# Optimization experiments

Measured on AMD Instinct MI355X. Metric: run time of the kernel, lower is better.

Reference implementation:

```python
import jax, jax.numpy as jnp
import numpy as np

B, N, MA, MB = 8, 16384, 256, 64
K_INTERP, K_AB = 3, 16


def _pn3(x, layers):
    # shared MLP over points: x [B, C, N]
    for w, b in layers:
        x = jax.nn.relu(jnp.einsum('oi,bin->bon', w, x) + b[None, :, None])
    return x


def _pn4(x, layers):
    # shared MLP over (node, neighbor): x [B, C, M, K]
    for w, b in layers:
        x = jax.nn.relu(jnp.einsum('oi,bimk->bomk', w, x) + b[None, :, None, None])
    return x


def _seg_sum(data, ids):  # data [B, N, C], ids [B, N] -> [B, MA, C]
    return jax.vmap(lambda d, i: jax.ops.segment_sum(d, i, num_segments=MA))(data, ids)


def _seg_max(data, ids):  # data [B, N, C], ids [B, N] -> [B, MA, C]
    return jax.vmap(lambda d, i: jax.ops.segment_max(d, i, num_segments=MA))(data, ids)


def _forward(pc, intensity, sn, label, node_a, node_b, *params):
    p = list(params)
    fp1 = [(p[0], p[1]), (p[2], p[3]), (p[4], p[5])]
    fp2 = [(p[6], p[7]), (p[8], p[9])]
    knn1 = [(p[10], p[11]), (p[12], p[13])]
    knn2 = [(p[14], p[15]), (p[16], p[17])]
    fin = [(p[18], p[19]), (p[20], p[21])]

    # ---- point -> node_a assignment (nearest node) ----
    diff = jnp.linalg.norm(pc[:, :, :, None] - node_a[:, :, None, :], axis=1)  # [B, N, MA]
    _, min_k_idx = jax.lax.top_k(-diff, K_INTERP)  # [B, N, k], smallest distances
    min_idx = min_k_idx[:, :, 0]  # [B, N]

    # ---- masked cluster mean (scatter-add by cluster id) ----
    counts = _seg_sum(jnp.ones((B, N, 1), pc.dtype), min_idx)[..., 0]  # [B, MA]
    nonempty = counts > 0  # mask_row_max
    cluster_mean = jnp.swapaxes(_seg_sum(jnp.swapaxes(pc, 1, 2), min_idx), 1, 2) / (counts[:, None, :] + 1e-5)  # [B,3,MA]

    pc_centers = jnp.take_along_axis(cluster_mean, jnp.broadcast_to(min_idx[:, None, :], (B, 3, N)), axis=2)
    pc_decentered = jax.lax.stop_gradient(pc - pc_centers)
    pc_aug = jnp.concatenate([pc_decentered, intensity, sn, label], axis=1)  # [B, 8, N]

    # ---- first PointNet + scatter-max fusion ----
    f1 = _pn3(pc_aug, fp1)  # [B, Ca/2, N]
    m1 = jnp.where(nonempty[:, None, :], jnp.swapaxes(_seg_max(jnp.swapaxes(f1, 1, 2), min_idx), 1, 2), 0.0)  # [B, Ca/2, MA]
    scat1 = jnp.take_along_axis(m1, jnp.broadcast_to(min_idx[:, None, :], (B, m1.shape[1], N)), axis=2)
    f2 = _pn3(jnp.concatenate([f1, scat1], axis=1), fp2)  # [B, Ca, N]
    node_a_features = jnp.where(nonempty[:, None, :], jnp.swapaxes(_seg_max(jnp.swapaxes(f2, 1, 2), min_idx), 1, 2), 0.0)  # [B, Ca, MA]

    # ---- KNN fusion: node_b queries vs cluster means ----
    d2 = jnp.linalg.norm(node_b[:, :, :, None] - cluster_mean[:, :, None, :], axis=1)  # [B, MB, MA]
    _, knn_idx = jax.lax.top_k(-d2, K_AB)  # [B, MB, K]
    pos_knn = jax.vmap(lambda cm, idx: cm[:, idx])(cluster_mean, knn_idx)  # [B, 3, MB, K]
    feat_knn = jax.vmap(lambda f, idx: f[:, idx])(node_a_features, knn_idx)  # [B, Ca, MB, K]
    x = jnp.concatenate([pos_knn - node_b[:, :, :, None], feat_knn], axis=1)  # [B, 3+Ca, MB, K]
    y = _pn4(x, knn1)  # [B, Cb, MB, K]
    pooled = jnp.max(y, axis=3, keepdims=True)
    z = _pn4(jnp.concatenate([jnp.broadcast_to(pooled, y.shape), y], axis=1), knn2)  # [B, Cb, MB, K]
    node_b_features = jnp.max(z, axis=3)  # [B, Cb, MB]

    # ---- final PointNet + global max-pool ----
    final = _pn3(jnp.concatenate([node_b, node_b_features], axis=1), fin)  # [B, Cg, MB]
    global_feature = jnp.max(final, axis=2, keepdims=True)  # [B, Cg, 1]
    return (pc_centers, cluster_mean, min_k_idx, f1, f2, node_a_features, node_b_features, global_feature)


def setup_inputs() -> dict:
    key = jax.random.key(0)
    ks = jax.random.split(key, 32)
    inp = {
        'pc': jax.random.normal(ks[0], (B, 3, N), jnp.float32),
        'intensity': jax.random.uniform(ks[1], (B, 1, N), dtype=jnp.float32),
        'sn': jax.random.normal(ks[2], (B, 3, N), jnp.float32),
        'label': jax.random.uniform(ks[3], (B, 1, N), dtype=jnp.float32),
        'node_a': jax.random.normal(ks[4], (B, 3, MA), jnp.float32),
        'node_b': jax.random.normal(ks[5], (B, 3, MB), jnp.float32),
    }
    i = [6]
    def lin(cin, cout):
        w = jax.random.normal(ks[i[0]], (cout, cin), jnp.float32) / np.sqrt(cin).astype(np.float32)
        i[0] += 1
        return w, jnp.zeros((cout,), jnp.float32)
    for name, dims in [('fp1', [8, 32, 32, 32]), ('fp2', [64, 64, 64]), ('knn1', [67, 256, 256]), ('knn2', [512, 512, 256]), ('fin', [259, 512, 1024])]:
        for j in range(len(dims) - 1):
            w, b = lin(dims[j], dims[j + 1])
            inp[f'{name}_w{j}'] = w
            inp[f'{name}_b{j}'] = b
    return inp


def reference(pc, intensity, sn, label, node_a, node_b, fp1_w0, fp1_b0, fp1_w1, fp1_b1, fp1_w2, fp1_b2, fp2_w0, fp2_b0, fp2_w1, fp2_b1, knn1_w0, knn1_b0, knn1_w1, knn1_b1, knn2_w0, knn2_b0, knn2_w1, knn2_b1, fin_w0, fin_b0, fin_w1, fin_b1):
    return _forward(pc, intensity, sn, label, node_a, node_b, fp1_w0, fp1_b0, fp1_w1, fp1_b1, fp1_w2, fp1_b2, fp2_w0, fp2_b0, fp2_w1, fp2_b1, knn1_w0, knn1_b0, knn1_w1, knn1_b1, knn2_w0, knn2_b0, knn2_w1, knn2_b1, fin_w0, fin_b0, fin_w1, fin_b1)
```

## Files before the change

kernel.cpp:

```cpp
#include <hip/hip_runtime.h>
#include <cstdint>
#include <cstddef>

#define B_   8
#define N_   16384
#define MA_  256
#define MB_  64
#define KI_  3
#define KAB_ 16

#define OFF_PCC 0
#define OFF_CM  393216
#define OFF_MKI 399360
#define OFF_F1  792576
#define OFF_F2  4986880
#define OFF_NAF 13375488
#define OFF_NBF 13506560
#define OFF_GF  13637632

__global__ __launch_bounds__(256) void k_top3(
    const float* __restrict__ pc, const float* __restrict__ node_a,
    float* __restrict__ out_mki, int* __restrict__ minidx,
    float* __restrict__ counts, float* __restrict__ sums)
{
#pragma clang fp contract(off)
    __shared__ float nax[MA_], nay[MA_], naz[MA_];
    int b = blockIdx.y;
    const float* na = node_a + (size_t)b * 3 * MA_;
    for (int t = threadIdx.x; t < MA_; t += 256) {
        nax[t] = na[t]; nay[t] = na[MA_ + t]; naz[t] = na[2 * MA_ + t];
    }
    __syncthreads();
    int n = blockIdx.x * 256 + threadIdx.x;
    const float* pcb = pc + (size_t)b * 3 * N_;
    float px = pcb[n], py = pcb[N_ + n], pz = pcb[2 * N_ + n];
    float d0 = 3.4e38f, d1 = 3.4e38f, d2 = 3.4e38f;
    int   i0 = 0, i1 = 0, i2 = 0;
    for (int m = 0; m < MA_; ++m) {
        float dx = px - nax[m];
        float dy = py - nay[m];
        float dz = pz - naz[m];
        float s = dx * dx;
        s = s + dy * dy;
        s = s + dz * dz;
        float d = sqrtf(s);
        if (d < d2) {
            if (d < d1) {
                if (d < d0) { d2 = d1; i2 = i1; d1 = d0; i1 = i0; d0 = d; i0 = m; }
                else        { d2 = d1; i2 = i1; d1 = d;  i1 = m; }
            } else          { d2 = d;  i2 = m; }
        }
    }
    size_t base = ((size_t)b * N_ + n) * 3;
    out_mki[base + 0] = (float)i0;
    out_mki[base + 1] = (float)i1;
    out_mki[base + 2] = (float)i2;
    minidx[b * N_ + n] = i0;
    atomicAdd(&counts[b * MA_ + i0], 1.0f);
    atomicAdd(&sums[(b * 3 + 0) * MA_ + i0], px);
    atomicAdd(&sums[(b * 3 + 1) * MA_ + i0], py);
    atomicAdd(&sums[(b * 3 + 2) * MA_ + i0], pz);
}

__global__ void k_mean(const float* __restrict__ counts, const float* __restrict__ sums,
                       float* __restrict__ out_cm)
{
    int tid = blockIdx.x * 256 + threadIdx.x;
    int b = tid >> 8, m = tid & 255;
    float den = counts[tid] + 1e-5f;
    #pragma unroll
    for (int c = 0; c < 3; ++c)
        out_cm[(b * 3 + c) * MA_ + m] = sums[(b * 3 + c) * MA_ + m] / den;
}

__global__ __launch_bounds__(256) void k_fp1(
    const float* __restrict__ pc, const float* __restrict__ inten,
    const float* __restrict__ sn, const float* __restrict__ label,
    const int* __restrict__ minidx, const float* __restrict__ cm,
    const float* __restrict__ w0, const float* __restrict__ b0,
    const float* __restrict__ w1, const float* __restrict__ b1,
    const float* __restrict__ w2, const float* __restrict__ b2,
    float* __restrict__ out_pcc, float* __restrict__ f1out)
{
    __shared__ float w0s[32 * 8], w1s[32 * 32], w2s[32 * 32];
    __shared__ float b0s[32], b1s[32], b2s[32];
    for (int t = threadIdx.x; t < 256; t += 256) w0s[t] = w0[t];
    for (int t = threadIdx.x; t < 1024; t += 256) { w1s[t] = w1[t]; w2s[t] = w2[t]; }
    if (threadIdx.x < 32) {
        b0s[threadIdx.x] = b0[threadIdx.x];
        b1s[threadIdx.x] = b1[threadIdx.x];
        b2s[threadIdx.x] = b2[threadIdx.x];
    }
    __syncthreads();
    int b = blockIdx.y;
    int n = blockIdx.x * 256 + threadIdx.x;
    int mi = minidx[b * N_ + n];
    float cx = cm[(b * 3 + 0) * MA_ + mi];
    float cy = cm[(b * 3 + 1) * MA_ + mi];
    float cz = cm[(b * 3 + 2) * MA_ + mi];
    const float* pcb = pc + (size_t)b * 3 * N_;
    const float* snb = sn + (size_t)b * 3 * N_;
    float x[8];
    x[0] = pcb[n] - cx; x[1] = pcb[N_ + n] - cy; x[2] = pcb[2 * N_ + n] - cz;
    x[3] = inten[(size_t)b * N_ + n];
    x[4] = snb[n]; x[5] = snb[N_ + n]; x[6] = snb[2 * N_ + n];
    x[7] = label[(size_t)b * N_ + n];
    out_pcc[(size_t)(b * 3 + 0) * N_ + n] = cx;
    out_pcc[(size_t)(b * 3 + 1) * N_ + n] = cy;
    out_pcc[(size_t)(b * 3 + 2) * N_ + n] = cz;

    float h1[32];
    #pragma unroll
    for (int o = 0; o < 32; ++o) {
        float a = b0s[o];
        #pragma unroll
        for (int i = 0; i < 8; ++i) a = fmaf(w0s[o * 8 + i], x[i], a);
        h1[o] = a > 0.f ? a : 0.f;
    }
    float h2[32];
    #pragma unroll
    for (int o = 0; o < 32; ++o) {
        float a = b1s[o];
        #pragma unroll
        for (int i = 0; i < 32; ++i) a = fmaf(w1s[o * 32 + i], h1[i], a);
        h2[o] = a > 0.f ? a : 0.f;
    }
    #pragma unroll
    for (int o = 0; o < 32; ++o) {
        float a = b2s[o];
        #pragma unroll
        for (int i = 0; i < 32; ++i) a = fmaf(w2s[o * 32 + i], h2[i], a);
        a = a > 0.f ? a : 0.f;
        f1out[(size_t)(b * 32 + o) * N_ + n] = a;
    }
}

__global__ __launch_bounds__(256) void k_segmax(
    const float* __restrict__ f, const int* __restrict__ minidx,
    float* __restrict__ outt, int F)
{
    __shared__ int table[MA_];
    int blk = blockIdx.x;
    int b = blk / F;
    table[threadIdx.x] = 0;
    __syncthreads();
    const float* frow = f + (size_t)blk * N_;
    const int*   mrow = minidx + (size_t)b * N_;
    #pragma unroll 4
    for (int it = 0; it < N_ / 256; ++it) {
        int n = it * 256 + threadIdx.x;
        float v = frow[n];
        int  mi = mrow[n];
        atomicMax(&table[mi], __float_as_int(v));
    }
    __syncthreads();
    outt[(size_t)blk * MA_ + threadIdx.x] = __int_as_float(table[threadIdx.x]);
}

__global__ __launch_bounds__(256) void k_fp2(
    const float* __restrict__ f1, const float* __restrict__ m1,
    const int* __restrict__ minidx,
    const float* __restrict__ w0, const float* __restrict__ b0,
    const float* __restrict__ w1, const float* __restrict__ b1,
    float* __restrict__ f2out)
{
    __shared__ float w0t[64 * 65];
    __shared__ float w1s[64 * 64];
    __shared__ float b0s[64], b1s[64];
    for (int t = threadIdx.x; t < 4096; t += 256) {
        w0t[(t & 63) * 65 + (t >> 6)] = w0[t];
        w1s[t] = w1[t];
    }
    if (threadIdx.x < 64) {
        b0s[threadIdx.x] = b0[threadIdx.x];
        b1s[threadIdx.x] = b1[threadIdx.x];
    }
    __syncthreads();
    int b = blockIdx.y;
    int n = blockIdx.x * 256 + threadIdx.x;
    int mi = minidx[b * N_ + n];

    float h[64];
    #pragma unroll
    for (int o = 0; o < 64; ++o) h[o] = b0s[o];
    for (int i = 0; i < 32; ++i) {
        float xi = f1[(size_t)(b * 32 + i) * N_ + n];
        #pragma unroll
        for (int o = 0; o < 64; ++o) h[o] = fmaf(w0t[i * 65 + o], xi, h[o]);
    }
    for (int i = 0; i < 32; ++i) {
        float xi = m1[(b * 32 + i) * MA_ + mi];
        #pragma unroll
        for (int o = 0; o < 64; ++o) h[o] = fmaf(w0t[(32 + i) * 65 + o], xi, h[o]);
    }
    #pragma unroll
    for (int o = 0; o < 64; ++o) h[o] = h[o] > 0.f ? h[o] : 0.f;

    for (int o2 = 0; o2 < 64; ++o2) {
        float acc = b1s[o2];
        #pragma unroll
        for (int i = 0; i < 64; ++i) acc = fmaf(w1s[o2 * 64 + i], h[i], acc);
        acc = acc > 0.f ? acc : 0.f;
        f2out[(size_t)(b * 64 + o2) * N_ + n] = acc;
    }
}

__global__ void k_knn16(const float* __restrict__ cm, const float* __restrict__ nb,
                        int* __restrict__ knnidx)
{
#pragma clang fp contract(off)
    __shared__ float dist[MA_];
    int blk = blockIdx.x;
    int b = blk >> 6, mb = blk & 63;
    float nbx = nb[(b * 3 + 0) * MB_ + mb];
    float nby = nb[(b * 3 + 1) * MB_ + mb];
    float nbz = nb[(b * 3 + 2) * MB_ + mb];
    for (int m = threadIdx.x; m < MA_; m += 64) {
        float dx = nbx - cm[(b * 3 + 0) * MA_ + m];
        float dy = nby - cm[(b * 3 + 1) * MA_ + m];
        float dz = nbz - cm[(b * 3 + 2) * MA_ + m];
        float s = dx * dx;
        s = s + dy * dy;
        s = s + dz * dz;
        dist[m] = sqrtf(s);
    }
    __syncthreads();
    if (threadIdx.x == 0) {
        for (int k = 0; k < KAB_; ++k) {
            float best = 3.4e38f; int bi = 0;
            for (int m = 0; m < MA_; ++m) {
                float d = dist[m];
                if (d < best) { best = d; bi = m; }
            }
            knnidx[blk * KAB_ + k] = bi;
            dist[bi] = 3.4e38f;
        }
    }
}

__global__ void k_buildx(const int* __restrict__ knnidx, const float* __restrict__ cm,
                         const float* __restrict__ nb, const float* __restrict__ naf,
                         float* __restrict__ Xk)
{
    int col = blockIdx.x * 256 + threadIdx.x;
    int b = col >> 10;
    int mb = (col >> 4) & 63;
    int idx = knnidx[col];
    #pragma unroll
    for (int c = 0; c < 3; ++c)
        Xk[(size_t)c * 8192 + col] = cm[(b * 3 + c) * MA_ + idx] - nb[(b * 3 + c) * MB_ + mb];
    for (int f = 0; f < 64; ++f)
        Xk[(size_t)(3 + f) * 8192 + col] = naf[(b * 64 + f) * MA_ + idx];
}

__global__ __launch_bounds__(256) void gemm_relu(
    const float* __restrict__ W, const float* __restrict__ bias,
    const float* __restrict__ X, float* __restrict__ Y,
    int O, int I, int C)
{
    __shared__ float Ws[16][64];
    __shared__ float Xs[16][64];
    int t  = threadIdx.x;
    int tx = t & 15, ty = t >> 4;
    int obase = blockIdx.y * 64;
    int cbase = blockIdx.x * 64;
    float acc[4][4] = {};
    for (int k0 = 0; k0 < I; k0 += 16) {
        {
            int m = t >> 2, kq = (t & 3) * 4;
            const float* wrow = W + (size_t)(obase + m) * I + k0 + kq;
            #pragma unroll
            for (int j = 0; j < 4; ++j) {
                int kk = kq + j;
                Ws[kk][m] = (k0 + kk < I) ? wrow[j] : 0.f;
            }
            int kx = t >> 4, nq = (t & 15) * 4;
            const float* xrow = X + (size_t)(k0 + kx) * C + cbase + nq;
            bool kok = (k0 + kx) < I;
            #pragma unroll
            for (int j = 0; j < 4; ++j)
                Xs[kx][nq + j] = kok ? xrow[j] : 0.f;
        }
        __syncthreads();
        #pragma unroll
        for (int kk = 0; kk < 16; ++kk) {
            float4 av = *(const float4*)&Ws[kk][ty * 4];
            float4 bv = *(const float4*)&Xs[kk][tx * 4];
            float am[4] = {av.x, av.y, av.z, av.w};
            float bn[4] = {bv.x, bv.y, bv.z, bv.w};
            #pragma unroll
            for (int i = 0; i < 4; ++i)
                #pragma unroll
                for (int j = 0; j < 4; ++j)
                    acc[i][j] = fmaf(am[i], bn[j], acc[i][j]);
        }
        __syncthreads();
    }
    #pragma unroll
    for (int i = 0; i < 4; ++i) {
        int o = obase + ty * 4 + i;
        float bb = bias[o];
        #pragma unroll
        for (int j = 0; j < 4; ++j) {
            int c = cbase + tx * 4 + j;
            float v = acc[i][j] + bb;
            Y[(size_t)o * C + c] = v > 0.f ? v : 0.f;
        }
    }
}

__global__ void k_pool(const float* __restrict__ Yk2, float* __restrict__ pooled)
{
    int tid = blockIdx.x * 256 + threadIdx.x;
    int r = tid >> 9, g = tid & 511;
    const float* p = Yk2 + (size_t)r * 8192 + g * 16;
    float m = p[0];
    #pragma unroll
    for (int k = 1; k < 16; ++k) m = fmaxf(m, p[k]);
    pooled[r * 512 + g] = m;
}

__global__ void k_zin(const float* __restrict__ pooled, const float* __restrict__ Yk2,
                      float* __restrict__ Zin)
{
    int tid = blockIdx.x * 256 + threadIdx.x;
    int r = tid >> 13, c = tid & 8191;
    float v = (r < 256) ? pooled[r * 512 + (c >> 4)]
                        : Yk2[(size_t)(r - 256) * 8192 + c];
    Zin[tid] = v;
}

__global__ void k_maxk(const float* __restrict__ Z2, float* __restrict__ nbf)
{
    int tid = blockIdx.x * 256 + threadIdx.x;
    int mb = tid & 63;
    int o  = (tid >> 6) & 255;
    int b  = tid >> 14;
    const float* p = Z2 + (size_t)o * 8192 + (size_t)((b * 64 + mb) << 4);
    float m = p[0];
    #pragma unroll
    for (int k = 1; k < 16; ++k) m = fmaxf(m, p[k]);
    nbf[tid] = m;
}

__global__ void k_finx(const float* __restrict__ nb, const float* __restrict__ nbf,
                       float* __restrict__ FinX)
{
    int tid = blockIdx.x * 256 + threadIdx.x;
    if (tid >= 259 * 512) return;
    int col = tid & 511, r = tid >> 9;
    int b = col >> 6, mb = col & 63;
    float v = (r < 3) ? nb[(b * 3 + r) * MB_ + mb]
                      : nbf[(b * 256 + (r - 3)) * MB_ + mb];
    FinX[tid] = v;
}

__global__ void k_gmax(const float* __restrict__ F2, float* __restrict__ gf)
{
    int tid = blockIdx.x * 256 + threadIdx.x;
    int b = tid >> 10, o = tid & 1023;
    const float* p = F2 + (size_t)o * 512 + b * 64;
    float m = p[0];
    #pragma unroll
    for (int k = 1; k < 64; ++k) m = fmaxf(m, p[k]);
    gf[tid] = m;
}

extern "C" void kernel_launch(void* const* d_in, const int* in_sizes, int n_in,
                              void* d_out, int out_size, void* d_ws, size_t ws_size,
                              hipStream_t stream)
{
    (void)in_sizes; (void)n_in; (void)out_size; (void)ws_size;
    const float* pc      = (const float*)d_in[0];
    const float* inten   = (const float*)d_in[1];
    const float* sn      = (const float*)d_in[2];
    const float* label   = (const float*)d_in[3];
    const float* node_a  = (const float*)d_in[4];
    const float* node_b  = (const float*)d_in[5];
    const float* fp1_w0  = (const float*)d_in[6];
    const float* fp1_b0  = (const float*)d_in[7];
    const float* fp1_w1  = (const float*)d_in[8];
    const float* fp1_b1  = (const float*)d_in[9];
    const float* fp1_w2  = (const float*)d_in[10];
    const float* fp1_b2  = (const float*)d_in[11];
    const float* fp2_w0  = (const float*)d_in[12];
    const float* fp2_b0  = (const float*)d_in[13];
    const float* fp2_w1  = (const float*)d_in[14];
    const float* fp2_b1  = (const float*)d_in[15];
    const float* knn1_w0 = (const float*)d_in[16];
    const float* knn1_b0 = (const float*)d_in[17];
    const float* knn1_w1 = (const float*)d_in[18];
    const float* knn1_b1 = (const float*)d_in[19];
    const float* knn2_w0 = (const float*)d_in[20];
    const float* knn2_b0 = (const float*)d_in[21];
    const float* knn2_w1 = (const float*)d_in[22];
    const float* knn2_b1 = (const float*)d_in[23];
    const float* fin_w0  = (const float*)d_in[24];
    const float* fin_b0  = (const float*)d_in[25];
    const float* fin_w1  = (const float*)d_in[26];
    const float* fin_b1  = (const float*)d_in[27];
    float* out = (float*)d_out;

    float* wsf    = (float*)d_ws;
    int*   minidx = (int*)wsf;
    float* counts = wsf + 131072;
    float* sums   = counts + 2048;
    float* m1     = sums + 6144;
    int*   knnidx = (int*)(m1 + 65536);
    float* Xk     = (float*)(knnidx + 8192);
    float* Yk1    = Xk + 548864;
    float* Yk2    = Yk1 + 2097152;
    float* pooled = Yk2 + 2097152;
    float* Zin    = pooled + 131072;
    float* Z1     = Zin + 4194304;
    float* Z2   = Yk1;
    float* FinX = Xk;
    float* F1   = Xk + 132608;
    float* F2   = Zin;

    hipMemsetAsync(counts, 0, (2048 + 6144) * sizeof(float), stream);

    k_top3<<<dim3(64, 8), 256, 0, stream>>>(pc, node_a, out + OFF_MKI, minidx, counts, sums);
    k_mean<<<8, 256, 0, stream>>>(counts, sums, out + OFF_CM);
    k_fp1<<<dim3(64, 8), 256, 0, stream>>>(pc, inten, sn, label, minidx, out + OFF_CM,
                                           fp1_w0, fp1_b0, fp1_w1, fp1_b1, fp1_w2, fp1_b2,
                                           out + OFF_PCC, out + OFF_F1);
    k_segmax<<<8 * 32, 256, 0, stream>>>(out + OFF_F1, minidx, m1, 32);
    k_fp2<<<dim3(64, 8), 256, 0, stream>>>(out + OFF_F1, m1, minidx,
                                           fp2_w0, fp2_b0, fp2_w1, fp2_b1,
                                           out + OFF_F2);
    k_segmax<<<8 * 64, 256, 0, stream>>>(out + OFF_F2, minidx, out + OFF_NAF, 64);
    k_knn16<<<512, 64, 0, stream>>>(out + OFF_CM, node_b, knnidx);
    k_buildx<<<32, 256, 0, stream>>>(knnidx, out + OFF_CM, node_b, out + OFF_NAF, Xk);
    gemm_relu<<<dim3(128, 4), 256, 0, stream>>>(knn1_w0, knn1_b0, Xk, Yk1, 256, 67, 8192);
    gemm_relu<<<dim3(128, 4), 256, 0, stream>>>(knn1_w1, knn1_b1, Yk1, Yk2, 256, 256, 8192);
    k_pool<<<512, 256, 0, stream>>>(Yk2, pooled);
    k_zin<<<16384, 256, 0, stream>>>(pooled, Yk2, Zin);
    gemm_relu<<<dim3(128, 8), 256, 0, stream>>>(knn2_w0, knn2_b0, Zin, Z1, 512, 512, 8192);
    gemm_relu<<<dim3(128, 4), 256, 0, stream>>>(knn2_w1, knn2_b1, Z1, Z2, 256, 512, 8192);
    k_maxk<<<512, 256, 0, stream>>>(Z2, out + OFF_NBF);
    k_finx<<<518, 256, 0, stream>>>(node_b, out + OFF_NBF, FinX);
    gemm_relu<<<dim3(8, 8), 256, 0, stream>>>(fin_w0, fin_b0, FinX, F1, 512, 259, 512);
    gemm_relu<<<dim3(8, 16), 256, 0, stream>>>(fin_w1, fin_b1, F1, F2, 1024, 512, 512);
    k_gmax<<<32, 256, 0, stream>>>(F2, out + OFF_GF);
}
```

Before: 698.8 us.

## Split knn2 first layer: apply pooled half once per group, drop concat buffer

The first knn2 layer takes as input the pooled features repeated over the 16 neighbors, concatenated with the per-neighbor features. It is split into two parts. A small GEMM applies the first 256 weight columns to the pooled features once per group. The main GEMM applies the remaining columns to Yk2 and adds the precomputed partial through a broadcast in the epilogue. This removes the k_zin concat kernel and its 16MB write, and halves the K dimension of the big GEMM. The cost is a new leading-dimension argument, a per-element gadd load, and a padded Ws shared tile.

```diff
diff --git a/kernel.cpp b/kernel.cpp
--- a/kernel.cpp
+++ b/kernel.cpp
@@ -256,9 +256,10 @@
 __global__ __launch_bounds__(256) void gemm_relu(
     const float* __restrict__ W, const float* __restrict__ bias,
     const float* __restrict__ X, float* __restrict__ Y,
-    int O, int I, int C)
-{
-    __shared__ float Ws[16][64];
+    int O, int I, int lda, int C,
+    const float* __restrict__ gadd, int do_relu)
+{
+    __shared__ float Ws[16][68];
     __shared__ float Xs[16][64];
     int t  = threadIdx.x;
     int tx = t & 15, ty = t >> 4;
@@ -268,7 +269,7 @@
     for (int k0 = 0; k0 < I; k0 += 16) {
         {
             int m = t >> 2, kq = (t & 3) * 4;
-            const float* wrow = W + (size_t)(obase + m) * I + k0 + kq;
+            const float* wrow = W + (size_t)(obase + m) * lda + k0 + kq;
             #pragma unroll
             for (int j = 0; j < 4; ++j) {
                 int kk = kq + j;
@@ -299,12 +300,14 @@
     #pragma unroll
     for (int i = 0; i < 4; ++i) {
         int o = obase + ty * 4 + i;
-        float bb = bias[o];
+        float bb = bias ? bias[o] : 0.f;
         #pragma unroll
         for (int j = 0; j < 4; ++j) {
             int c = cbase + tx * 4 + j;
             float v = acc[i][j] + bb;
-            Y[(size_t)o * C + c] = v > 0.f ? v : 0.f;
+            if (gadd) v += gadd[(size_t)o * 512 + (c >> 4)];
+            if (do_relu) v = v > 0.f ? v : 0.f;
+            Y[(size_t)o * C + c] = v;
         }
     }
 }
@@ -318,16 +321,6 @@
     #pragma unroll
     for (int k = 1; k < 16; ++k) m = fmaxf(m, p[k]);
     pooled[r * 512 + g] = m;
-}
-
-__global__ void k_zin(const float* __restrict__ pooled, const float* __restrict__ Yk2,
-                      float* __restrict__ Zin)
-{
-    int tid = blockIdx.x * 256 + threadIdx.x;
-    int r = tid >> 13, c = tid & 8191;
-    float v = (r < 256) ? pooled[r * 512 + (c >> 4)]
-                        : Yk2[(size_t)(r - 256) * 8192 + c];
-    Zin[tid] = v;
 }
 
 __global__ void k_maxk(const float* __restrict__ Z2, float* __restrict__ nbf)
@@ -411,12 +404,12 @@
     float* Yk1    = Xk + 548864;
     float* Yk2    = Yk1 + 2097152;
     float* pooled = Yk2 + 2097152;
-    float* Zin    = pooled + 131072;
-    float* Z1     = Zin + 4194304;
+    float* Ppart  = pooled + 131072;
+    float* Z1     = Ppart + 4194304;
     float* Z2   = Yk1;
     float* FinX = Xk;
     float* F1   = Xk + 132608;
-    float* F2   = Zin;
+    float* F2   = Ppart + 262144;
 
     hipMemsetAsync(counts, 0, (2048 + 6144) * sizeof(float), stream);
 
@@ -432,15 +425,22 @@
     k_segmax<<<8 * 64, 256, 0, stream>>>(out + OFF_F2, minidx, out + OFF_NAF, 64);
     k_knn16<<<512, 64, 0, stream>>>(out + OFF_CM, node_b, knnidx);
     k_buildx<<<32, 256, 0, stream>>>(knnidx, out + OFF_CM, node_b, out + OFF_NAF, Xk);
-    gemm_relu<<<dim3(128, 4), 256, 0, stream>>>(knn1_w0, knn1_b0, Xk, Yk1, 256, 67, 8192);
-    gemm_relu<<<dim3(128, 4), 256, 0, stream>>>(knn1_w1, knn1_b1, Yk1, Yk2, 256, 256, 8192);
+    gemm_relu<<<dim3(128, 4), 256, 0, stream>>>(knn1_w0, knn1_b0, Xk, Yk1,
+                                                256, 67, 67, 8192, nullptr, 1);
+    gemm_relu<<<dim3(128, 4), 256, 0, stream>>>(knn1_w1, knn1_b1, Yk1, Yk2,
+                                                256, 256, 256, 8192, nullptr, 1);
     k_pool<<<512, 256, 0, stream>>>(Yk2, pooled);
-    k_zin<<<16384, 256, 0, stream>>>(pooled, Yk2, Zin);
-    gemm_relu<<<dim3(128, 8), 256, 0, stream>>>(knn2_w0, knn2_b0, Zin, Z1, 512, 512, 8192);
-    gemm_relu<<<dim3(128, 4), 256, 0, stream>>>(knn2_w1, knn2_b1, Z1, Z2, 256, 512, 8192);
+    gemm_relu<<<dim3(8, 8), 256, 0, stream>>>(knn2_w0, nullptr, pooled, Ppart,
+                                              512, 256, 512, 512, nullptr, 0);
+    gemm_relu<<<dim3(128, 8), 256, 0, stream>>>(knn2_w0 + 256, knn2_b0, Yk2, Z1,
+                                                512, 256, 512, 8192, Ppart, 1);
+    gemm_relu<<<dim3(128, 4), 256, 0, stream>>>(knn2_w1, knn2_b1, Z1, Z2,
+                                                256, 512, 512, 8192, nullptr, 1);
     k_maxk<<<512, 256, 0, stream>>>(Z2, out + OFF_NBF);
     k_finx<<<518, 256, 0, stream>>>(node_b, out + OFF_NBF, FinX);
-    gemm_relu<<<dim3(8, 8), 256, 0, stream>>>(fin_w0, fin_b0, FinX, F1, 512, 259, 512);
-    gemm_relu<<<dim3(8, 16), 256, 0, stream>>>(fin_w1, fin_b1, F1, F2, 1024, 512, 512);
+    gemm_relu<<<dim3(8, 8), 256, 0, stream>>>(fin_w0, fin_b0, FinX, F1,
+                                              512, 259, 259, 512, nullptr, 1);
+    gemm_relu<<<dim3(8, 16), 256, 0, stream>>>(fin_w1, fin_b1, F1, F2,
+                                               1024, 512, 512, 512, nullptr, 1);
     k_gmax<<<32, 256, 0, stream>>>(F2, out + OFF_GF);
 }
```

Measured after the change: 698.8 us. Within noise of the previous version (+0.0%).
